# Kernel optimization log

Measured on AMD Instinct MI355X. Metric: run time of the kernel, lower is better.

Reference implementation:

```python
import jax, jax.numpy as jnp
import numpy as np
from functools import partial

H = 768
E = 1536
B = 4
L = 4096

def layer_norm(x, g, b, eps=1e-5):
    mu = jnp.mean(x, axis=-1, keepdims=True)
    var = jnp.mean((x - mu) ** 2, axis=-1, keepdims=True)
    return (x - mu) * jax.lax.rsqrt(var + eps) * g + b

def l2_normalize(x, eps=1e-12):
    n = jnp.sqrt(jnp.sum(x * x, axis=-1, keepdims=True))
    return x / jnp.maximum(n, eps)

def dw_conv(x, w):
    # x: [B, L, E], w: [E, 1, 3] depthwise kernel (torch Conv1d groups=E layout)
    y = jax.lax.conv_general_dilated(
        x.transpose(0, 2, 1), w, window_strides=(1,), padding=[(1, 1)],
        dimension_numbers=('NCH', 'OIH', 'NCH'), feature_group_count=E)
    return y.transpose(0, 2, 1)

def setup_inputs() -> dict:
    key = jax.random.key(0)
    ks = jax.random.split(key, 12)
    d = {}
    d['x'] = jax.random.normal(ks[0], (B, L, H), jnp.float32)
    d['ln1_g'] = jnp.ones((H,), jnp.float32)
    d['ln1_b'] = jnp.zeros((H,), jnp.float32)
    d['ln2_g'] = jnp.ones((E,), jnp.float32)
    d['ln2_b'] = jnp.zeros((E,), jnp.float32)
    d['W_in'] = 0.02 * jax.random.normal(ks[1], (3 * E, H), jnp.float32)
    d['b_in'] = jnp.zeros((3 * E,), jnp.float32)
    d['W_beta'] = jnp.zeros((E, H), jnp.float32)  # torch init: constant 0
    d['b_beta'] = jnp.ones((E,), jnp.float32)     # torch init: constant 1
    d['W_out'] = 0.02 * jax.random.normal(ks[2], (H, E), jnp.float32)
    d['b_out'] = jnp.zeros((H,), jnp.float32)
    d['W1'] = 0.02 * jax.random.normal(ks[3], (4 * H, H), jnp.float32)
    d['b1'] = jnp.zeros((4 * H,), jnp.float32)
    d['W2'] = 0.02 * jax.random.normal(ks[4], (H, 4 * H), jnp.float32)
    d['b2'] = jnp.zeros((H,), jnp.float32)
    d['conv_w'] = jax.random.normal(ks[5], (E, 1, 3), jnp.float32) / jnp.sqrt(3.0)
    d['attn_scale'] = jnp.ones((1,), jnp.float32)
    return d

def reference(x, ln1_g, ln1_b, ln2_g, ln2_b, W_in, b_in, W_beta, b_beta,
              W_out, b_out, W1, b1, W2, b2, conv_w, attn_scale):
    shortcut = x
    xn = layer_norm(x, ln1_g, ln1_b)
    qkv = xn @ W_in.T + b_in
    q, k, v = jnp.split(qkv, 3, axis=-1)
    q = jax.nn.silu(q)
    k = jax.nn.silu(k)
    v = jax.nn.gelu(v, approximate=False)
    q = l2_normalize(q) + 0.1 * k
    k = l2_normalize(k) + 0.1 * q
    q = dw_conv(q, conv_w)
    k = dw_conv(k, conv_w)
    v = dw_conv(v, conv_w)
    beta = jax.nn.sigmoid(xn @ W_beta.T + b_beta) * 0.9 + 0.1
    # initial state is zero, so v_old = 0 and v_new = beta * v (same math as torch code)
    v_new = beta * v                                   # [B, L, E]
    state = jnp.einsum('ble,blf->bef', v_new, k)       # v_new^T @ k : [B, E, E]
    out = jnp.einsum('blf,bef->ble', q, state)         # q @ state^T
    out = out * attn_scale
    out = layer_norm(out, ln2_g, ln2_b)
    out = out @ W_out.T + b_out
    x = shortcut + out
    h = layer_norm(x, ln1_g, ln1_b)
    h = jax.nn.gelu(h @ W1.T + b1, approximate=False) @ W2.T + b2
    return x + h
```

## Files before the change

kernel.cpp:

```cpp
#include <hip/hip_runtime.h>
#include <hip/hip_bf16.h>
#include <cstdint>
#include <cstddef>

using bf16_t = __hip_bfloat16;
typedef __bf16 bf16x8 __attribute__((ext_vector_type(8)));
typedef __bf16 bf16x4 __attribute__((ext_vector_type(4)));
typedef float f32x4 __attribute__((ext_vector_type(4)));

#define DEVI static __device__ __forceinline__

DEVI float b2f(bf16_t v) { return __bfloat162float(v); }
DEVI bf16_t f2b(float v) { return __float2bfloat16(v); }

DEVI float fsigmoid(float x) { return 1.0f / (1.0f + __expf(-x)); }
DEVI float fsilu(float x) { return x * fsigmoid(x); }
DEVI float fgelu(float x) { return 0.5f * x * (1.0f + erff(x * 0.70710678118654752440f)); }

DEVI void g2l16(const bf16_t* g, bf16_t* l) {
    __builtin_amdgcn_global_load_lds(
        (const __attribute__((address_space(1))) void*)g,
        (__attribute__((address_space(3))) void*)l,
        16, 0, 0);
}

template<int ACT, bool RESID, bool OUTBF, bool QKVSPLIT>
__global__ __launch_bounds__(256) void gemm_nt(
    const bf16_t* __restrict__ A, const bf16_t* __restrict__ B,
    void* __restrict__ Cout, const float* __restrict__ bias,
    const float* __restrict__ resid,
    int M, int N, int K, long long sA, long long sB, long long sC)
{
    __shared__ bf16_t As[128 * 32];
    __shared__ bf16_t Bs[128 * 32];

    const int t  = threadIdx.x;
    const int w  = t >> 6;
    const int ln = t & 63;
    const long long bz = blockIdx.z;
    A += bz * sA;
    B += bz * sB;
    const long long cbase = QKVSPLIT ? 0 : bz * sC;

    const int m0 = blockIdx.y * 128;
    const int n0 = blockIdx.x * 128;
    const int wm = (w >> 1) * 64;
    const int wn = (w & 1) * 64;

    f32x4 acc[4][4] = {};

    const int rI0 = (w * 2 + 0) * 16 + (ln >> 2);
    const int rI1 = (w * 2 + 1) * 16 + (ln >> 2);
    const int kc8 = (((ln & 3) ^ ((ln >> 3) & 3)) * 8);
    bf16_t* ldsA0 = &As[(w * 2 + 0) * 512];
    bf16_t* ldsA1 = &As[(w * 2 + 1) * 512];
    bf16_t* ldsB0 = &Bs[(w * 2 + 0) * 512];
    bf16_t* ldsB1 = &Bs[(w * 2 + 1) * 512];

    const int fr = ln & 15;
    const int koff = (((ln >> 4) ^ ((ln >> 1) & 3)) * 8);

    for (int k0 = 0; k0 < K; k0 += 32) {
        g2l16(A + (size_t)(m0 + rI0) * K + k0 + kc8, ldsA0);
        g2l16(A + (size_t)(m0 + rI1) * K + k0 + kc8, ldsA1);
        g2l16(B + (size_t)(n0 + rI0) * K + k0 + kc8, ldsB0);
        g2l16(B + (size_t)(n0 + rI1) * K + k0 + kc8, ldsB1);
        __syncthreads();

        bf16x8 af[4], bfr[4];
#pragma unroll
        for (int i = 0; i < 4; ++i) {
            af[i]  = *(const bf16x8*)&As[(wm + i * 16 + fr) * 32 + koff];
            bfr[i] = *(const bf16x8*)&Bs[(wn + i * 16 + fr) * 32 + koff];
        }
#pragma unroll
        for (int mi = 0; mi < 4; ++mi)
#pragma unroll
            for (int ni = 0; ni < 4; ++ni)
                acc[mi][ni] = __builtin_amdgcn_mfma_f32_16x16x32_bf16(
                    bfr[ni], af[mi], acc[mi][ni], 0, 0, 0);
        __syncthreads();
    }

    const int rb = (ln >> 4) * 4;
    f32x4 bias4[4];
#pragma unroll
    for (int ni = 0; ni < 4; ++ni) {
        f32x4 z = {};
        bias4[ni] = bias ? *(const f32x4*)&bias[n0 + wn + ni * 16 + rb] : z;
    }
#pragma unroll
    for (int mi = 0; mi < 4; ++mi) {
        const int row = m0 + wm + mi * 16 + fr;
#pragma unroll
        for (int ni = 0; ni < 4; ++ni) {
            const int col0 = n0 + wn + ni * 16 + rb;
            f32x4 v = acc[mi][ni] + bias4[ni];
            if constexpr (ACT == 1) {
#pragma unroll
                for (int r = 0; r < 4; ++r) v[r] = fgelu(v[r]);
            }
            long long off;
            if constexpr (QKVSPLIT) {
                const int seg = col0 / 1536;
                off = (long long)seg * sC + (long long)row * 1536
                    + (col0 - seg * 1536);
            } else {
                off = cbase + (long long)row * N + col0;
            }
            if constexpr (RESID) v += *(const f32x4*)&resid[off];
            if constexpr (OUTBF) {
                bf16x4 o;
#pragma unroll
                for (int r = 0; r < 4; ++r) o[r] = (__bf16)v[r];
                *(bf16x4*)((bf16_t*)Cout + off) = o;
            } else {
                *(f32x4*)((float*)Cout + off) = v;
            }
        }
    }
}

template<int NT>
__global__ __launch_bounds__(NT) void ln_v4(
    const float* __restrict__ x, const float* __restrict__ g,
    const float* __restrict__ b, bf16_t* __restrict__ out,
    const float* __restrict__ scale_ptr)
{
    constexpr int n = NT * 4;
    constexpr int NW = NT / 64;
    const int row = blockIdx.x, t = threadIdx.x;
    const float scale = scale_ptr ? scale_ptr[0] : 1.0f;
    f32x4 v = *(const f32x4*)&x[(size_t)row * n + t * 4];
    v *= scale;
    float s  = v[0] + v[1] + v[2] + v[3];
    float ss = v[0]*v[0] + v[1]*v[1] + v[2]*v[2] + v[3]*v[3];
#pragma unroll
    for (int m = 32; m; m >>= 1) { s += __shfl_xor(s, m, 64); ss += __shfl_xor(ss, m, 64); }
    __shared__ float red[2 * NW];
    const int w = t >> 6;
    if ((t & 63) == 0) { red[w] = s; red[NW + w] = ss; }
    __syncthreads();
    s = 0.f; ss = 0.f;
#pragma unroll
    for (int i = 0; i < NW; ++i) { s += red[i]; ss += red[NW + i]; }
    const float mean = s / n;
    const float rstd = rsqrtf(ss / n - mean * mean + 1e-5f);
    const f32x4 gv = *(const f32x4*)&g[t * 4];
    const f32x4 bv = *(const f32x4*)&b[t * 4];
    bf16x4 o;
#pragma unroll
    for (int r = 0; r < 4; ++r)
        o[r] = (__bf16)((v[r] - mean) * rstd * gv[r] + bv[r]);
    *(bf16x4*)&out[(size_t)row * n + t * 4] = o;
}

__global__ __launch_bounds__(192) void qk_norms(
    const bf16_t* __restrict__ q, const bf16_t* __restrict__ k,
    float2* __restrict__ norms)
{
    const int row = blockIdx.x, t = threadIdx.x;
    const bf16x8 q8 = *(const bf16x8*)&q[(size_t)row * 1536 + t * 8];
    const bf16x8 k8 = *(const bf16x8*)&k[(size_t)row * 1536 + t * 8];
    float sq = 0.f, sk = 0.f;
#pragma unroll
    for (int i = 0; i < 8; ++i) {
        const float a = fsilu((float)q8[i]);
        const float c = fsilu((float)k8[i]);
        sq += a * a; sk += c * c;
    }
#pragma unroll
    for (int m = 32; m; m >>= 1) { sq += __shfl_xor(sq, m, 64); sk += __shfl_xor(sk, m, 64); }
    __shared__ float red[6];
    const int w = t >> 6;
    if ((t & 63) == 0) { red[w] = sq; red[3 + w] = sk; }
    __syncthreads();
    if (t == 0) {
        sq = red[0] + red[1] + red[2];
        sk = red[3] + red[4] + red[5];
        float2 o;
        o.x = 1.0f / fmaxf(sqrtf(sq), 1e-12f);
        o.y = 1.0f / fmaxf(sqrtf(sk), 1e-12f);
        norms[row] = o;
    }
}

template<int STREAM>
__global__ __launch_bounds__(256) void act_conv(
    const bf16_t* __restrict__ src0,
    const bf16_t* __restrict__ src1,
    const float2* __restrict__ norms,
    bf16_t* __restrict__ dst, const float* __restrict__ cw)
{
    constexpr int L = 4096, E = 1536;
    const int b = blockIdx.z;
    const int e0 = blockIdx.x * 128, l0 = blockIdx.y * 64;
    const int t = threadIdx.x;
    const int le = t & 15, lt = t >> 4;
    const int e = e0 + le * 8;
    const int lbase = l0 + lt * 4;
    const size_t rowL = (size_t)b * L;

    float w0[8], w1[8], w2[8];
#pragma unroll
    for (int i = 0; i < 8; ++i) {
        w0[i] = cw[(e + i) * 3 + 0];
        w1[i] = cw[(e + i) * 3 + 1];
        w2[i] = cw[(e + i) * 3 + 2];
    }

    float s[6][8];
#pragma unroll
    for (int w = 0; w < 6; ++w) {
        const int l = lbase - 1 + w;
        if (l < 0 || l >= L) {
#pragma unroll
            for (int i = 0; i < 8; ++i) s[w][i] = 0.f;
            continue;
        }
        const size_t off = (rowL + l) * E + e;
        const bf16x8 a8 = *(const bf16x8*)&src0[off];
        if constexpr (STREAM == 2) {
#pragma unroll
            for (int i = 0; i < 8; ++i) s[w][i] = fgelu((float)a8[i]);
        } else {
            const bf16x8 k8 = *(const bf16x8*)&src1[off];
            const float2 nm = norms[rowL + l];
#pragma unroll
            for (int i = 0; i < 8; ++i) {
                const float sq = fsilu((float)a8[i]);
                const float sk = fsilu((float)k8[i]);
                const float q1 = sq * nm.x + 0.1f * sk;
                s[w][i] = (STREAM == 0) ? q1 : (sk * nm.y + 0.1f * q1);
            }
        }
    }

    float o[4][8];
#pragma unroll
    for (int j = 0; j < 4; ++j)
#pragma unroll
        for (int i = 0; i < 8; ++i)
            o[j][i] = w0[i] * s[j][i] + w1[i] * s[j + 1][i] + w2[i] * s[j + 2][i];

    if constexpr (STREAM == 2) {
#pragma unroll
        for (int j = 0; j < 4; ++j) {
            const bf16x8 b8 = *(const bf16x8*)&src1[(rowL + lbase + j) * E + e];
#pragma unroll
            for (int i = 0; i < 8; ++i)
                o[j][i] *= fsigmoid((float)b8[i]) * 0.9f + 0.1f;
        }
    }

    if constexpr (STREAM == 0) {
#pragma unroll
        for (int j = 0; j < 4; ++j) {
            bf16x8 ov;
#pragma unroll
            for (int i = 0; i < 8; ++i) ov[i] = (__bf16)o[j][i];
            *(bf16x8*)&dst[(rowL + lbase + j) * E + e] = ov;
        }
    } else {
#pragma unroll
        for (int i = 0; i < 8; ++i) {
            bf16x4 ov;
#pragma unroll
            for (int j = 0; j < 4; ++j) ov[j] = (__bf16)o[j][i];
            *(bf16x4*)&dst[((size_t)b * E + e + i) * L + lbase] = ov;
        }
    }
}

__global__ __launch_bounds__(256) void cast_f2b_v4(
    const float* __restrict__ src, bf16_t* __restrict__ dst, int n4)
{
    const int i = blockIdx.x * 256 + threadIdx.x;
    if (i < n4) {
        const f32x4 v = ((const f32x4*)src)[i];
        bf16x4 o;
#pragma unroll
        for (int r = 0; r < 4; ++r) o[r] = (__bf16)v[r];
        ((bf16x4*)dst)[i] = o;
    }
}

__global__ void diag_ws(float* o, float v) { o[threadIdx.x] = v; }


extern "C" void kernel_launch(void* const* d_in, const int* in_sizes, int n_in,
                              void* d_out, int out_size, void* d_ws, size_t ws_size,
                              hipStream_t stream)
{
    constexpr int B = 4, L = 4096, H = 768, E = 1536;
    constexpr int T = B * L;
    constexpr size_t SEGE = (size_t)T * E;
    constexpr size_t S    = SEGE * 2;
    constexpr size_t o_bcat  = 5 * S;
    constexpr size_t o_norms = o_bcat + 6144 * 4;
    constexpr size_t WS_NEED = o_norms + (size_t)T * 8;

    const float* x       = (const float*)d_in[0];
    const float* ln1_g   = (const float*)d_in[1];
    const float* ln1_b   = (const float*)d_in[2];
    const float* ln2_g   = (const float*)d_in[3];
    const float* ln2_b   = (const float*)d_in[4];
    const float* W_in    = (const float*)d_in[5];
    const float* b_in    = (const float*)d_in[6];
    const float* W_beta  = (const float*)d_in[7];
    const float* b_beta  = (const float*)d_in[8];
    const float* W_out   = (const float*)d_in[9];
    const float* b_out   = (const float*)d_in[10];
    const float* W1      = (const float*)d_in[11];
    const float* b1      = (const float*)d_in[12];
    const float* W2      = (const float*)d_in[13];
    const float* b2      = (const float*)d_in[14];
    const float* conv_w  = (const float*)d_in[15];
    const float* attn_sc = (const float*)d_in[16];

    if (ws_size < WS_NEED) {
        diag_ws<<<1, 256, 0, stream>>>((float*)d_out,
                                       10000.0f + (float)(ws_size >> 20));
        return;
    }

    char* ws = (char*)d_ws;
    bf16_t* slotA = (bf16_t*)(ws + 0 * S);
    bf16_t* slotB = (bf16_t*)(ws + 1 * S);
    bf16_t* slotC = (bf16_t*)(ws + 2 * S);
    bf16_t* slotD = (bf16_t*)(ws + 3 * S);
    bf16_t* slotE = (bf16_t*)(ws + 4 * S);
    float*  bcat  = (float*)(ws + o_bcat);
    float2* norms = (float2*)(ws + o_norms);

    bf16_t* Wcat = slotE;
    bf16_t* xn   = (bf16_t*)((char*)slotE + (size_t)6144 * H * 2);

    bf16_t* vT    = slotE;
    bf16_t* kT    = slotC;
    bf16_t* qc    = slotD;
    bf16_t* state = slotA;
    float*  attn  = (float*)slotB;
    bf16_t* ln2o  = slotE;
    bf16_t* WoutB = (bf16_t*)((char*)slotB + (size_t)28 * 1024 * 1024);
    bf16_t* W1B   = (bf16_t*)((char*)WoutB + (size_t)H * E * 2);
    bf16_t* W2B   = (bf16_t*)((char*)W1B + (size_t)4 * H * H * 2);
    float*  x2    = (float*)slotA;
    bf16_t* xn2   = slotB;
    bf16_t* h1    = slotC;

    auto cast = [&](const float* s, bf16_t* d, int n) {
        cast_f2b_v4<<<(n / 4 + 255) / 256, 256, 0, stream>>>(s, d, n / 4);
    };

    cast(W_in,   Wcat,                     3 * E * H);
    cast(W_beta, Wcat + (size_t)3 * E * H, E * H);
    hipMemcpyAsync(bcat,         b_in,   3 * E * sizeof(float), hipMemcpyDeviceToDevice, stream);
    hipMemcpyAsync(bcat + 3 * E, b_beta, E * sizeof(float),     hipMemcpyDeviceToDevice, stream);

    ln_v4<192><<<T, 192, 0, stream>>>(x, ln1_g, ln1_b, xn, nullptr);

    gemm_nt<0, false, true, true><<<dim3(6144 / 128, T / 128, 1), 256, 0, stream>>>(
        xn, Wcat, slotA, bcat, nullptr, T, 6144, H, 0, 0, (long long)SEGE);

    qk_norms<<<T, 192, 0, stream>>>(slotA, slotB, norms);

    act_conv<2><<<dim3(E / 128, L / 64, B), 256, 0, stream>>>(slotC, slotD, nullptr, vT, conv_w);
    act_conv<1><<<dim3(E / 128, L / 64, B), 256, 0, stream>>>(slotA, slotB, norms, kT, conv_w);
    act_conv<0><<<dim3(E / 128, L / 64, B), 256, 0, stream>>>(slotA, slotB, norms, qc, conv_w);

    gemm_nt<0, false, true, false><<<dim3(E / 128, E / 128, B), 256, 0, stream>>>(
        vT, kT, state, nullptr, nullptr, E, E, L,
        (long long)E * L, (long long)E * L, (long long)E * E);

    gemm_nt<0, false, false, false><<<dim3(E / 128, L / 128, B), 256, 0, stream>>>(
        qc, state, attn, nullptr, nullptr, L, E, E,
        (long long)L * E, (long long)E * E, (long long)L * E);

    ln_v4<384><<<T, 384, 0, stream>>>(attn, ln2_g, ln2_b, ln2o, attn_sc);

    cast(W_out, WoutB, H * E);
    cast(W1,    W1B,   4 * H * H);
    cast(W2,    W2B,   H * 4 * H);

    gemm_nt<0, true, false, false><<<dim3(H / 128, T / 128, 1), 256, 0, stream>>>(
        ln2o, WoutB, x2, b_out, x, T, H, E, 0, 0, 0);

    ln_v4<192><<<T, 192, 0, stream>>>(x2, ln1_g, ln1_b, xn2, nullptr);

    gemm_nt<1, false, true, false><<<dim3(4 * H / 128, T / 128, 1), 256, 0, stream>>>(
        xn2, W1B, h1, b1, nullptr, T, 4 * H, H, 0, 0, 0);

    gemm_nt<0, true, false, false><<<dim3(H / 128, T / 128, 1), 256, 0, stream>>>(
        h1, W2B, (float*)d_out, b2, x2, T, H, 4 * H, 0, 0, 0);
}
```

Baseline: 1.213 ms.

## Widen GEMM K-tile, fuse activations into QKV epilogue, merge prep casts

```diff
diff --git a/kernel.cpp b/kernel.cpp
--- a/kernel.cpp
+++ b/kernel.cpp
@@ -11,7 +11,6 @@
 #define DEVI static __device__ __forceinline__
 
 DEVI float b2f(bf16_t v) { return __bfloat162float(v); }
-DEVI bf16_t f2b(float v) { return __float2bfloat16(v); }
 
 DEVI float fsigmoid(float x) { return 1.0f / (1.0f + __expf(-x)); }
 DEVI float fsilu(float x) { return x * fsigmoid(x); }
@@ -31,8 +30,8 @@
     const float* __restrict__ resid,
     int M, int N, int K, long long sA, long long sB, long long sC)
 {
-    __shared__ bf16_t As[128 * 32];
-    __shared__ bf16_t Bs[128 * 32];
+    __shared__ bf16_t As[128 * 64];
+    __shared__ bf16_t Bs[128 * 64];
 
     const int t  = threadIdx.x;
     const int w  = t >> 6;
@@ -49,29 +48,49 @@
 
     f32x4 acc[4][4] = {};
 
-    const int rI0 = (w * 2 + 0) * 16 + (ln >> 2);
-    const int rI1 = (w * 2 + 1) * 16 + (ln >> 2);
-    const int kc8 = (((ln & 3) ^ ((ln >> 3) & 3)) * 8);
-    bf16_t* ldsA0 = &As[(w * 2 + 0) * 512];
-    bf16_t* ldsA1 = &As[(w * 2 + 1) * 512];
-    bf16_t* ldsB0 = &Bs[(w * 2 + 0) * 512];
-    bf16_t* ldsB1 = &Bs[(w * 2 + 1) * 512];
+    const int sr = ln >> 3;
+    const int sc = (ln & 7) ^ sr;
+    const bf16_t* Ap = A + (size_t)(m0 + w * 32 + sr) * K + sc * 8;
+    const bf16_t* Bp = B + (size_t)(n0 + w * 32 + sr) * K + sc * 8;
+    bf16_t* ldsA = &As[(w * 32) * 64];
+    bf16_t* ldsB = &Bs[(w * 32) * 64];
 
     const int fr = ln & 15;
-    const int koff = (((ln >> 4) ^ ((ln >> 1) & 3)) * 8);
-
-    for (int k0 = 0; k0 < K; k0 += 32) {
-        g2l16(A + (size_t)(m0 + rI0) * K + k0 + kc8, ldsA0);
-        g2l16(A + (size_t)(m0 + rI1) * K + k0 + kc8, ldsA1);
-        g2l16(B + (size_t)(n0 + rI0) * K + k0 + kc8, ldsB0);
-        g2l16(B + (size_t)(n0 + rI1) * K + k0 + kc8, ldsB1);
+    const int qd = ln >> 4;
+    int roA[4], roB[4];
+#pragma unroll
+    for (int i = 0; i < 4; ++i) {
+        roA[i] = (wm + i * 16 + fr) * 64;
+        roB[i] = (wn + i * 16 + fr) * 64;
+    }
+    const int so0 = ((qd)     ^ (fr & 7)) * 8;
+    const int so1 = ((4 + qd) ^ (fr & 7)) * 8;
+
+    for (int k0 = 0; k0 < K; k0 += 64) {
+#pragma unroll
+        for (int i = 0; i < 4; ++i) {
+            g2l16(Ap + (size_t)(i * 8) * K, ldsA + (i * 8) * 64);
+            g2l16(Bp + (size_t)(i * 8) * K, ldsB + (i * 8) * 64);
+        }
+        Ap += 64; Bp += 64;
         __syncthreads();
 
         bf16x8 af[4], bfr[4];
 #pragma unroll
         for (int i = 0; i < 4; ++i) {
-            af[i]  = *(const bf16x8*)&As[(wm + i * 16 + fr) * 32 + koff];
-            bfr[i] = *(const bf16x8*)&Bs[(wn + i * 16 + fr) * 32 + koff];
+            af[i]  = *(const bf16x8*)&As[roA[i] + so0];
+            bfr[i] = *(const bf16x8*)&Bs[roB[i] + so0];
+        }
+#pragma unroll
+        for (int mi = 0; mi < 4; ++mi)
+#pragma unroll
+            for (int ni = 0; ni < 4; ++ni)
+                acc[mi][ni] = __builtin_amdgcn_mfma_f32_16x16x32_bf16(
+                    bfr[ni], af[mi], acc[mi][ni], 0, 0, 0);
+#pragma unroll
+        for (int i = 0; i < 4; ++i) {
+            af[i]  = *(const bf16x8*)&As[roA[i] + so1];
+            bfr[i] = *(const bf16x8*)&Bs[roB[i] + so1];
         }
 #pragma unroll
         for (int mi = 0; mi < 4; ++mi)
@@ -82,7 +101,8 @@
         __syncthreads();
     }
 
-    const int rb = (ln >> 4) * 4;
+    const int rb = qd * 4;
+    const int seg = QKVSPLIT ? (n0 / 1536) : 0;
     f32x4 bias4[4];
 #pragma unroll
     for (int ni = 0; ni < 4; ++ni) {
@@ -100,9 +120,20 @@
 #pragma unroll
                 for (int r = 0; r < 4; ++r) v[r] = fgelu(v[r]);
             }
+            if constexpr (ACT == 3) {
+                if (seg <= 1) {
+#pragma unroll
+                    for (int r = 0; r < 4; ++r) v[r] = fsilu(v[r]);
+                } else if (seg == 2) {
+#pragma unroll
+                    for (int r = 0; r < 4; ++r) v[r] = fgelu(v[r]);
+                } else {
+#pragma unroll
+                    for (int r = 0; r < 4; ++r) v[r] = fsigmoid(v[r]) * 0.9f + 0.1f;
+                }
+            }
             long long off;
             if constexpr (QKVSPLIT) {
-                const int seg = col0 / 1536;
                 off = (long long)seg * sC + (long long)row * 1536
                     + (col0 - seg * 1536);
             } else {
@@ -124,15 +155,12 @@
 template<int NT>
 __global__ __launch_bounds__(NT) void ln_v4(
     const float* __restrict__ x, const float* __restrict__ g,
-    const float* __restrict__ b, bf16_t* __restrict__ out,
-    const float* __restrict__ scale_ptr)
+    const float* __restrict__ b, bf16_t* __restrict__ out)
 {
     constexpr int n = NT * 4;
     constexpr int NW = NT / 64;
     const int row = blockIdx.x, t = threadIdx.x;
-    const float scale = scale_ptr ? scale_ptr[0] : 1.0f;
     f32x4 v = *(const f32x4*)&x[(size_t)row * n + t * 4];
-    v *= scale;
     float s  = v[0] + v[1] + v[2] + v[3];
     float ss = v[0]*v[0] + v[1]*v[1] + v[2]*v[2] + v[3]*v[3];
 #pragma unroll
@@ -155,6 +183,44 @@
     *(bf16x4*)&out[(size_t)row * n + t * 4] = o;
 }
 
+__global__ __launch_bounds__(192) void ln_bf16_1536(
+    const bf16_t* __restrict__ x, const float* __restrict__ g,
+    const float* __restrict__ b, bf16_t* __restrict__ out,
+    const float* __restrict__ scale_ptr)
+{
+    const int row = blockIdx.x, t = threadIdx.x;
+    const float scale = scale_ptr[0];
+    const bf16x8 x8 = *(const bf16x8*)&x[(size_t)row * 1536 + t * 8];
+    float v[8];
+    float s = 0.f, ss = 0.f;
+#pragma unroll
+    for (int i = 0; i < 8; ++i) {
+        v[i] = (float)x8[i] * scale;
+        s += v[i]; ss += v[i] * v[i];
+    }
+#pragma unroll
+    for (int m = 32; m; m >>= 1) { s += __shfl_xor(s, m, 64); ss += __shfl_xor(ss, m, 64); }
+    __shared__ float red[6];
+    const int w = t >> 6;
+    if ((t & 63) == 0) { red[w] = s; red[3 + w] = ss; }
+    __syncthreads();
+    s  = red[0] + red[1] + red[2];
+    ss = red[3] + red[4] + red[5];
+    const float mean = s / 1536.f;
+    const float rstd = rsqrtf(ss / 1536.f - mean * mean + 1e-5f);
+    const f32x4 g0 = *(const f32x4*)&g[t * 8];
+    const f32x4 g1 = *(const f32x4*)&g[t * 8 + 4];
+    const f32x4 b0 = *(const f32x4*)&b[t * 8];
+    const f32x4 b1 = *(const f32x4*)&b[t * 8 + 4];
+    bf16x8 o;
+#pragma unroll
+    for (int r = 0; r < 4; ++r) {
+        o[r]     = (__bf16)((v[r]     - mean) * rstd * g0[r] + b0[r]);
+        o[r + 4] = (__bf16)((v[r + 4] - mean) * rstd * g1[r] + b1[r]);
+    }
+    *(bf16x8*)&out[(size_t)row * 1536 + t * 8] = o;
+}
+
 __global__ __launch_bounds__(192) void qk_norms(
     const bf16_t* __restrict__ q, const bf16_t* __restrict__ k,
     float2* __restrict__ norms)
@@ -165,8 +231,8 @@
     float sq = 0.f, sk = 0.f;
 #pragma unroll
     for (int i = 0; i < 8; ++i) {
-        const float a = fsilu((float)q8[i]);
-        const float c = fsilu((float)k8[i]);
+        const float a = (float)q8[i];
+        const float c = (float)k8[i];
         sq += a * a; sk += c * c;
     }
 #pragma unroll
@@ -185,104 +251,163 @@
     }
 }
 
-template<int STREAM>
-__global__ __launch_bounds__(256) void act_conv(
-    const bf16_t* __restrict__ src0,
-    const bf16_t* __restrict__ src1,
+__global__ __launch_bounds__(256) void ac_qk(
+    const bf16_t* __restrict__ qs, const bf16_t* __restrict__ ks,
     const float2* __restrict__ norms,
-    bf16_t* __restrict__ dst, const float* __restrict__ cw)
+    bf16_t* __restrict__ qc, bf16_t* __restrict__ kT,
+    const float* __restrict__ cw)
 {
     constexpr int L = 4096, E = 1536;
     const int b = blockIdx.z;
-    const int e0 = blockIdx.x * 128, l0 = blockIdx.y * 64;
+    const int e0 = blockIdx.x * 64, l0 = blockIdx.y * 64;
     const int t = threadIdx.x;
-    const int le = t & 15, lt = t >> 4;
-    const int e = e0 + le * 8;
-    const int lbase = l0 + lt * 4;
+    const int e = e0 + (t & 15) * 4;
+    const int lbase = l0 + (t >> 4) * 4;
     const size_t rowL = (size_t)b * L;
 
-    float w0[8], w1[8], w2[8];
-#pragma unroll
-    for (int i = 0; i < 8; ++i) {
+    float w0[4], w1[4], w2[4];
+#pragma unroll
+    for (int i = 0; i < 4; ++i) {
         w0[i] = cw[(e + i) * 3 + 0];
         w1[i] = cw[(e + i) * 3 + 1];
         w2[i] = cw[(e + i) * 3 + 2];
     }
 
-    float s[6][8];
-#pragma unroll
-    for (int w = 0; w < 6; ++w) {
-        const int l = lbase - 1 + w;
+    float sq[6][4], sk[6][4];
+#pragma unroll
+    for (int j = 0; j < 6; ++j) {
+        const int l = lbase - 1 + j;
         if (l < 0 || l >= L) {
 #pragma unroll
-            for (int i = 0; i < 8; ++i) s[w][i] = 0.f;
+            for (int i = 0; i < 4; ++i) { sq[j][i] = 0.f; sk[j][i] = 0.f; }
             continue;
         }
         const size_t off = (rowL + l) * E + e;
-        const bf16x8 a8 = *(const bf16x8*)&src0[off];
-        if constexpr (STREAM == 2) {
-#pragma unroll
-            for (int i = 0; i < 8; ++i) s[w][i] = fgelu((float)a8[i]);
-        } else {
-            const bf16x8 k8 = *(const bf16x8*)&src1[off];
-            const float2 nm = norms[rowL + l];
-#pragma unroll
-            for (int i = 0; i < 8; ++i) {
-                const float sq = fsilu((float)a8[i]);
-                const float sk = fsilu((float)k8[i]);
-                const float q1 = sq * nm.x + 0.1f * sk;
-                s[w][i] = (STREAM == 0) ? q1 : (sk * nm.y + 0.1f * q1);
-            }
-        }
-    }
-
-    float o[4][8];
-#pragma unroll
-    for (int j = 0; j < 4; ++j)
-#pragma unroll
-        for (int i = 0; i < 8; ++i)
-            o[j][i] = w0[i] * s[j][i] + w1[i] * s[j + 1][i] + w2[i] * s[j + 2][i];
-
-    if constexpr (STREAM == 2) {
-#pragma unroll
-        for (int j = 0; j < 4; ++j) {
-            const bf16x8 b8 = *(const bf16x8*)&src1[(rowL + lbase + j) * E + e];
-#pragma unroll
-            for (int i = 0; i < 8; ++i)
-                o[j][i] *= fsigmoid((float)b8[i]) * 0.9f + 0.1f;
-        }
-    }
-
-    if constexpr (STREAM == 0) {
-#pragma unroll
-        for (int j = 0; j < 4; ++j) {
-            bf16x8 ov;
-#pragma unroll
-            for (int i = 0; i < 8; ++i) ov[i] = (__bf16)o[j][i];
-            *(bf16x8*)&dst[(rowL + lbase + j) * E + e] = ov;
-        }
+        const bf16x4 q4 = *(const bf16x4*)&qs[off];
+        const bf16x4 k4 = *(const bf16x4*)&ks[off];
+        const float2 nm = norms[rowL + l];
+#pragma unroll
+        for (int i = 0; i < 4; ++i) {
+            const float q1 = (float)q4[i] * nm.x + 0.1f * (float)k4[i];
+            const float k1 = (float)k4[i] * nm.y + 0.1f * q1;
+            sq[j][i] = q1; sk[j][i] = k1;
+        }
+    }
+
+#pragma unroll
+    for (int j = 0; j < 4; ++j) {
+        bf16x4 oq;
+#pragma unroll
+        for (int i = 0; i < 4; ++i)
+            oq[i] = (__bf16)(w0[i] * sq[j][i] + w1[i] * sq[j + 1][i] + w2[i] * sq[j + 2][i]);
+        *(bf16x4*)&qc[(rowL + lbase + j) * E + e] = oq;
+    }
+#pragma unroll
+    for (int i = 0; i < 4; ++i) {
+        bf16x4 ok;
+#pragma unroll
+        for (int j = 0; j < 4; ++j)
+            ok[j] = (__bf16)(w0[i] * sk[j][i] + w1[i] * sk[j + 1][i] + w2[i] * sk[j + 2][i]);
+        *(bf16x4*)&kT[((size_t)b * E + e + i) * L + lbase] = ok;
+    }
+}
+
+__global__ __launch_bounds__(256) void ac_v(
+    const bf16_t* __restrict__ vg, const bf16_t* __restrict__ beta,
+    bf16_t* __restrict__ vT, const float* __restrict__ cw)
+{
+    constexpr int L = 4096, E = 1536;
+    const int b = blockIdx.z;
+    const int e0 = blockIdx.x * 64, l0 = blockIdx.y * 64;
+    const int t = threadIdx.x;
+    const int e = e0 + (t & 15) * 4;
+    const int lbase = l0 + (t >> 4) * 4;
+    const size_t rowL = (size_t)b * L;
+
+    float w0[4], w1[4], w2[4];
+#pragma unroll
+    for (int i = 0; i < 4; ++i) {
+        w0[i] = cw[(e + i) * 3 + 0];
+        w1[i] = cw[(e + i) * 3 + 1];
+        w2[i] = cw[(e + i) * 3 + 2];
+    }
+
+    float s[6][4];
+#pragma unroll
+    for (int j = 0; j < 6; ++j) {
+        const int l = lbase - 1 + j;
+        if (l < 0 || l >= L) {
+#pragma unroll
+            for (int i = 0; i < 4; ++i) s[j][i] = 0.f;
+            continue;
+        }
+        const bf16x4 v4 = *(const bf16x4*)&vg[(rowL + l) * E + e];
+#pragma unroll
+        for (int i = 0; i < 4; ++i) s[j][i] = (float)v4[i];
+    }
+
+    float o[4][4];
+#pragma unroll
+    for (int j = 0; j < 4; ++j) {
+        const bf16x4 b4 = *(const bf16x4*)&beta[(rowL + lbase + j) * E + e];
+#pragma unroll
+        for (int i = 0; i < 4; ++i)
+            o[j][i] = (w0[i] * s[j][i] + w1[i] * s[j + 1][i] + w2[i] * s[j + 2][i])
+                      * (float)b4[i];
+    }
+#pragma unroll
+    for (int i = 0; i < 4; ++i) {
+        bf16x4 ov;
+#pragma unroll
+        for (int j = 0; j < 4; ++j) ov[j] = (__bf16)o[j][i];
+        *(bf16x4*)&vT[((size_t)b * E + e + i) * L + lbase] = ov;
+    }
+}
+
+__global__ __launch_bounds__(256) void prep1(
+    const float* __restrict__ Win, const float* __restrict__ Wbeta,
+    const float* __restrict__ bin, const float* __restrict__ bbeta,
+    bf16_t* __restrict__ Wcat, float* __restrict__ bcat)
+{
+    constexpr int nWin4 = 3 * 1536 * 768 / 4;
+    constexpr int nWb4  = 1536 * 768 / 4;
+    const int i = blockIdx.x * 256 + threadIdx.x;
+    if (i < nWin4) {
+        const f32x4 v = ((const f32x4*)Win)[i];
+        bf16x4 o;
+#pragma unroll
+        for (int r = 0; r < 4; ++r) o[r] = (__bf16)v[r];
+        ((bf16x4*)Wcat)[i] = o;
+    } else if (i < nWin4 + nWb4) {
+        const f32x4 v = ((const f32x4*)Wbeta)[i - nWin4];
+        bf16x4 o;
+#pragma unroll
+        for (int r = 0; r < 4; ++r) o[r] = (__bf16)v[r];
+        ((bf16x4*)Wcat)[i] = o;
     } else {
-#pragma unroll
-        for (int i = 0; i < 8; ++i) {
-            bf16x4 ov;
-#pragma unroll
-            for (int j = 0; j < 4; ++j) ov[j] = (__bf16)o[j][i];
-            *(bf16x4*)&dst[((size_t)b * E + e + i) * L + lbase] = ov;
-        }
-    }
-}
-
-__global__ __launch_bounds__(256) void cast_f2b_v4(
-    const float* __restrict__ src, bf16_t* __restrict__ dst, int n4)
-{
+        const int j = i - nWin4 - nWb4;
+        ((f32x4*)bcat)[j] = (j < 1152) ? ((const f32x4*)bin)[j]
+                                       : ((const f32x4*)bbeta)[j - 1152];
+    }
+}
+
+__global__ __launch_bounds__(256) void prep2(
+    const float* __restrict__ Wout, const float* __restrict__ W1,
+    const float* __restrict__ W2, bf16_t* __restrict__ dst)
+{
+    constexpr int n0 = 768 * 1536 / 4;
+    constexpr int n1 = n0 + 3072 * 768 / 4;
     const int i = blockIdx.x * 256 + threadIdx.x;
-    if (i < n4) {
-        const f32x4 v = ((const f32x4*)src)[i];
-        bf16x4 o;
-#pragma unroll
-        for (int r = 0; r < 4; ++r) o[r] = (__bf16)v[r];
-        ((bf16x4*)dst)[i] = o;
-    }
+    const float* src;
+    int j;
+    if (i < n0)      { src = Wout; j = i; }
+    else if (i < n1) { src = W1;   j = i - n0; }
+    else             { src = W2;   j = i - n1; }
+    const f32x4 v = ((const f32x4*)src)[j];
+    bf16x4 o;
+#pragma unroll
+    for (int r = 0; r < 4; ++r) o[r] = (__bf16)v[r];
+    ((bf16x4*)dst)[i] = o;
 }
 
 __global__ void diag_ws(float* o, float v) { o[threadIdx.x] = v; }
@@ -340,53 +465,43 @@
     bf16_t* kT    = slotC;
     bf16_t* qc    = slotD;
     bf16_t* state = slotA;
-    float*  attn  = (float*)slotB;
+    bf16_t* WoutB = (bf16_t*)((char*)slotA + (size_t)20 * 1024 * 1024);
+    bf16_t* W1B   = WoutB + (size_t)H * E;
+    bf16_t* W2B   = W1B + (size_t)4 * H * H;
+    bf16_t* attn  = slotB;
     bf16_t* ln2o  = slotE;
-    bf16_t* WoutB = (bf16_t*)((char*)slotB + (size_t)28 * 1024 * 1024);
-    bf16_t* W1B   = (bf16_t*)((char*)WoutB + (size_t)H * E * 2);
-    bf16_t* W2B   = (bf16_t*)((char*)W1B + (size_t)4 * H * H * 2);
-    float*  x2    = (float*)slotA;
+    float*  x2    = (float*)slotC;
     bf16_t* xn2   = slotB;
-    bf16_t* h1    = slotC;
-
-    auto cast = [&](const float* s, bf16_t* d, int n) {
-        cast_f2b_v4<<<(n / 4 + 255) / 256, 256, 0, stream>>>(s, d, n / 4);
-    };
-
-    cast(W_in,   Wcat,                     3 * E * H);
-    cast(W_beta, Wcat + (size_t)3 * E * H, E * H);
-    hipMemcpyAsync(bcat,         b_in,   3 * E * sizeof(float), hipMemcpyDeviceToDevice, stream);
-    hipMemcpyAsync(bcat + 3 * E, b_beta, E * sizeof(float),     hipMemcpyDeviceToDevice, stream);
-
-    ln_v4<192><<<T, 192, 0, stream>>>(x, ln1_g, ln1_b, xn, nullptr);
-
-    gemm_nt<0, false, true, true><<<dim3(6144 / 128, T / 128, 1), 256, 0, stream>>>(
+    bf16_t* h1    = slotD;
+
+    prep1<<<4614, 256, 0, stream>>>(W_in, W_beta, b_in, b_beta, Wcat, bcat);
+
+    ln_v4<192><<<T, 192, 0, stream>>>(x, ln1_g, ln1_b, xn);
+
+    gemm_nt<3, false, true, true><<<dim3(6144 / 128, T / 128, 1), 256, 0, stream>>>(
         xn, Wcat, slotA, bcat, nullptr, T, 6144, H, 0, 0, (long long)SEGE);
 
     qk_norms<<<T, 192, 0, stream>>>(slotA, slotB, norms);
 
-    act_conv<2><<<dim3(E / 128, L / 64, B), 256, 0, stream>>>(slotC, slotD, nullptr, vT, conv_w);
-    act_conv<1><<<dim3(E / 128, L / 64, B), 256, 0, stream>>>(slotA, slotB, norms, kT, conv_w);
-    act_conv<0><<<dim3(E / 128, L / 64, B), 256, 0, stream>>>(slotA, slotB, norms, qc, conv_w);
+    ac_v <<<dim3(E / 64, L / 64, B), 256, 0, stream>>>(slotC, slotD, vT, conv_w);
+    ac_qk<<<dim3(E / 64, L / 64, B), 256, 0, stream>>>(slotA, slotB, norms, qc, kT, conv_w);
+
+    prep2<<<5760, 256, 0, stream>>>(W_out, W1, W2, WoutB);
 
     gemm_nt<0, false, true, false><<<dim3(E / 128, E / 128, B), 256, 0, stream>>>(
         vT, kT, state, nullptr, nullptr, E, E, L,
         (long long)E * L, (long long)E * L, (long long)E * E);
 
-    gemm_nt<0, false, false, false><<<dim3(E / 128, L / 128, B), 256, 0, stream>>>(
+    gemm_nt<0, false, true, false><<<dim3(E / 128, L / 128, B), 256, 0, stream>>>(
         qc, state, attn, nullptr, nullptr, L, E, E,
         (long long)L * E, (long long)E * E, (long long)L * E);
 
-    ln_v4<384><<<T, 384, 0, stream>>>(attn, ln2_g, ln2_b, ln2o, attn_sc);
-
-    cast(W_out, WoutB, H * E);
-    cast(W1,    W1B,   4 * H * H);
-    cast(W2,    W2B,   H * 4 * H);
+    ln_bf16_1536<<<T, 192, 0, stream>>>(attn, ln2_g, ln2_b, ln2o, attn_sc);
 
     gemm_nt<0, true, false, false><<<dim3(H / 128, T / 128, 1), 256, 0, stream>>>(
         ln2o, WoutB, x2, b_out, x, T, H, E, 0, 0, 0);
 
-    ln_v4<192><<<T, 192, 0, stream>>>(x2, ln1_g, ln1_b, xn2, nullptr);
+    ln_v4<192><<<T, 192, 0, stream>>>(x2, ln1_g, ln1_b, xn2);
 
     gemm_nt<1, false, true, false><<<dim3(4 * H / 128, T / 128, 1), 256, 0, stream>>>(
         xn2, W1B, h1, b1, nullptr, T, 4 * H, H, 0, 0, 0);
```

New measurement: 1.090 ms. 10.1% less time.
